# Kernel optimization log

Measured on AMD Instinct MI355X. Metric: run time of the kernel, lower is better.

The kernel has to match this reference:

```python
import jax, jax.numpy as jnp
import numpy as np

B, S, E, H = 2, 2048, 512, 8
D = E // H  # head_dim = 64


def setup_inputs() -> dict:
    key = jax.random.key(0)
    ks = jax.random.split(key, 10)
    sc = 1.0 / np.sqrt(E)
    x = jax.random.normal(ks[0], (B, S, E), dtype=jnp.float32)
    # parent index per node: tree_structure[b][parent[b,i]] contains i
    parent = jax.random.randint(ks[1], (B, S), 0, S, dtype=jnp.int32)
    Wp = jax.random.normal(ks[2], (E, E), dtype=jnp.float32) * sc
    bp = jnp.zeros((E,), dtype=jnp.float32)
    Wc = jax.random.normal(ks[3], (E, E), dtype=jnp.float32) * sc
    bc = jnp.zeros((E,), dtype=jnp.float32)
    Ws = jax.random.normal(ks[4], (E, E), dtype=jnp.float32) * sc
    bs = jnp.zeros((E,), dtype=jnp.float32)
    Wo = jax.random.normal(ks[5], (E, E), dtype=jnp.float32) * sc
    bo = jnp.zeros((E,), dtype=jnp.float32)
    return {"x": x, "parent": parent, "Wp": Wp, "bp": bp, "Wc": Wc,
            "bc": bc, "Ws": Ws, "bs": bs, "Wo": Wo, "bo": bo}


def _tree_mask(parent):
    # Vectorized equivalent of the per-batch scatter loop:
    # mask[b, p, c] = mask[b, c, p] = 1 for each (parent, child) edge.
    b_idx = jnp.arange(B)[:, None]
    rows = jnp.arange(S)[None, :]
    m = jnp.zeros((B, S, S), dtype=bool)
    m = m.at[b_idx, rows, parent].set(True)
    m = m.at[b_idx, parent, rows].set(True)
    return m  # (B, S, S), broadcast over heads


def reference(x, parent, Wp, bp, Wc, bc, Ws, bs, Wo, bo):
    # Tri-projection
    p = (x @ Wp + bp).reshape(B, S, H, D)
    c = (x @ Wc + bc).reshape(B, S, H, D)
    s = (x @ Ws + bs).reshape(B, S, H, D)
    scores = jnp.einsum('bnhd,bmhd->bnhm', p, c) / jnp.sqrt(jnp.float32(D))
    mask = _tree_mask(parent)  # (B, S, S)
    scores = jnp.where(mask[:, :, None, :], scores, -jnp.inf)
    attn = jax.nn.softmax(scores, axis=-1)  # dropout is identity (train=False)
    out = jnp.einsum('bnhm,bmhd->bnhd', attn, s).reshape(B, S, E)
    return out @ Wo + bo
```

## Files before the change

### kernel.cpp

```cpp
#include <hip/hip_runtime.h>
#include <hip/hip_bf16.h>

#define B_  2
#define S_  2048
#define E_  512
#define H_  8
#define D_  64
#define BS_ (B_ * S_)
#define N1_ 1536
#define K_  512

typedef __bf16 bf16x8 __attribute__((ext_vector_type(8)));
typedef float  f32x4  __attribute__((ext_vector_type(4)));
typedef unsigned short us8 __attribute__((ext_vector_type(8)));

__device__ __forceinline__ ushort f2bf(float f) {
    unsigned u = __float_as_uint(f);
    unsigned r = (u + 0x7FFFu + ((u >> 16) & 1u)) >> 16;
    return (ushort)r;
}
__device__ __forceinline__ float bf2f(ushort b) {
    return __uint_as_float(((unsigned)b) << 16);
}

__device__ __forceinline__ void gld_lds16(const ushort* g, ushort* l) {
    __builtin_amdgcn_global_load_lds(
        (const __attribute__((address_space(1))) unsigned int*)g,
        (__attribute__((address_space(3))) unsigned int*)l, 16, 0, 0);
}

__global__ __launch_bounds__(256) void gemm1_kernel(
    const float* __restrict__ x,
    const float* __restrict__ Wp, const float* __restrict__ Wc,
    const float* __restrict__ Ws,
    const float* __restrict__ bp, const float* __restrict__ bc,
    const float* __restrict__ bs,
    ushort* __restrict__ PCS) {
    constexpr int TM = 128, TN = 96, TK = 64, LDP = 72;
    __shared__ ushort As[TM][LDP];
    __shared__ ushort Bs[TN][LDP];

    const int tid  = threadIdx.x;
    const int lane = tid & 63;
    const int wave = tid >> 6;
    const int wm = wave >> 1, wn = wave & 1;
    const int row0 = blockIdx.y * TM;
    const int col0 = blockIdx.x * TN;

    f32x4 acc[4][3] = {};

    const int ar  = tid >> 4;
    const int ac4 = tid & 15;
    const int lrow = lane & 15;
    const int lk   = (lane >> 4) * 8;

    for (int kt = 0; kt < K_; kt += TK) {
        #pragma unroll
        for (int j = 0; j < 8; j++) {
            int row = j * 16 + ar;
            float4 v = *(const float4*)(x + (size_t)(row0 + row) * K_ + kt + ac4 * 4);
            ushort4 h;
            h.x = f2bf(v.x); h.y = f2bf(v.y); h.z = f2bf(v.z); h.w = f2bf(v.w);
            *(ushort4*)(&As[row][ac4 * 4]) = h;
        }
        #pragma unroll
        for (int rd = 0; rd < 2; rd++) {
            int pid = rd * 256 + tid;
            if (pid < 384) {
                int pk = pid / 24, pn = pid % 24;
                int gc = col0 + pn * 4;
                const float* Wseg = (gc < 512) ? (Wp + gc)
                                  : (gc < 1024) ? (Wc + gc - 512)
                                  : (Ws + gc - 1024);
                float4 r0 = *(const float4*)(Wseg + (size_t)(kt + pk * 4 + 0) * 512);
                float4 r1 = *(const float4*)(Wseg + (size_t)(kt + pk * 4 + 1) * 512);
                float4 r2 = *(const float4*)(Wseg + (size_t)(kt + pk * 4 + 2) * 512);
                float4 r3 = *(const float4*)(Wseg + (size_t)(kt + pk * 4 + 3) * 512);
                ushort4 h;
                h.x = f2bf(r0.x); h.y = f2bf(r1.x); h.z = f2bf(r2.x); h.w = f2bf(r3.x);
                *(ushort4*)(&Bs[pn * 4 + 0][pk * 4]) = h;
                h.x = f2bf(r0.y); h.y = f2bf(r1.y); h.z = f2bf(r2.y); h.w = f2bf(r3.y);
                *(ushort4*)(&Bs[pn * 4 + 1][pk * 4]) = h;
                h.x = f2bf(r0.z); h.y = f2bf(r1.z); h.z = f2bf(r2.z); h.w = f2bf(r3.z);
                *(ushort4*)(&Bs[pn * 4 + 2][pk * 4]) = h;
                h.x = f2bf(r0.w); h.y = f2bf(r1.w); h.z = f2bf(r2.w); h.w = f2bf(r3.w);
                *(ushort4*)(&Bs[pn * 4 + 3][pk * 4]) = h;
            }
        }
        __syncthreads();

        #pragma unroll
        for (int kk = 0; kk < TK; kk += 32) {
            bf16x8 af[4], bfr[3];
            #pragma unroll
            for (int i = 0; i < 4; i++)
                af[i] = *(const bf16x8*)(&As[wm * 64 + i * 16 + lrow][kk + lk]);
            #pragma unroll
            for (int j = 0; j < 3; j++)
                bfr[j] = *(const bf16x8*)(&Bs[wn * 48 + j * 16 + lrow][kk + lk]);
            #pragma unroll
            for (int i = 0; i < 4; i++)
                #pragma unroll
                for (int j = 0; j < 3; j++)
                    acc[i][j] = __builtin_amdgcn_mfma_f32_16x16x32_bf16(
                        af[i], bfr[j], acc[i][j], 0, 0, 0);
        }
        __syncthreads();
    }

    const int ccol = lane & 15;
    const int crow = (lane >> 4) * 4;
    #pragma unroll
    for (int j = 0; j < 3; j++) {
        int gcol = col0 + wn * 48 + j * 16 + ccol;
        float bias = (gcol < 512) ? bp[gcol]
                   : (gcol < 1024) ? bc[gcol - 512] : bs[gcol - 1024];
        #pragma unroll
        for (int i = 0; i < 4; i++) {
            int grow = row0 + wm * 64 + i * 16 + crow;
            #pragma unroll
            for (int rg = 0; rg < 4; rg++)
                PCS[(size_t)(grow + rg) * N1_ + gcol] = f2bf(acc[i][j][rg] + bias);
        }
    }
}

__global__ __launch_bounds__(256) void gemm2_kernel(
    const ushort* __restrict__ A,
    const float* __restrict__ Wo, const float* __restrict__ bo,
    float* __restrict__ out) {
    constexpr int TM = 64, TN = 64, TK = 64, LDP = 72;
    __shared__ ushort As[TM][TK];
    __shared__ ushort Bs[TN][LDP];

    const int tid  = threadIdx.x;
    const int lane = tid & 63;
    const int wave = tid >> 6;
    const int wm = wave >> 1, wn = wave & 1;
    const int row0 = blockIdx.y * TM;
    const int col0 = blockIdx.x * TN;

    f32x4 acc[2][2] = {};

    const int srow = lane >> 3;
    const int scol = (lane & 7) * 8;
    const int pk = tid >> 4, pn = tid & 15;
    const int lrow = lane & 15;
    const int lk   = (lane >> 4) * 8;

    for (int kt = 0; kt < K_; kt += TK) {
        const ushort* ga = A + (size_t)(row0 + wave * 16 + srow) * K_ + kt + scol;
        gld_lds16(ga,            &As[wave * 16 + 0][0]);
        gld_lds16(ga + 8 * K_,   &As[wave * 16 + 8][0]);

        {
            const float* Wseg = Wo + col0 + pn * 4;
            float4 r0 = *(const float4*)(Wseg + (size_t)(kt + pk * 4 + 0) * 512);
            float4 r1 = *(const float4*)(Wseg + (size_t)(kt + pk * 4 + 1) * 512);
            float4 r2 = *(const float4*)(Wseg + (size_t)(kt + pk * 4 + 2) * 512);
            float4 r3 = *(const float4*)(Wseg + (size_t)(kt + pk * 4 + 3) * 512);
            ushort4 h;
            h.x = f2bf(r0.x); h.y = f2bf(r1.x); h.z = f2bf(r2.x); h.w = f2bf(r3.x);
            *(ushort4*)(&Bs[pn * 4 + 0][pk * 4]) = h;
            h.x = f2bf(r0.y); h.y = f2bf(r1.y); h.z = f2bf(r2.y); h.w = f2bf(r3.y);
            *(ushort4*)(&Bs[pn * 4 + 1][pk * 4]) = h;
            h.x = f2bf(r0.z); h.y = f2bf(r1.z); h.z = f2bf(r2.z); h.w = f2bf(r3.z);
            *(ushort4*)(&Bs[pn * 4 + 2][pk * 4]) = h;
            h.x = f2bf(r0.w); h.y = f2bf(r1.w); h.z = f2bf(r2.w); h.w = f2bf(r3.w);
            *(ushort4*)(&Bs[pn * 4 + 3][pk * 4]) = h;
        }
        __syncthreads();

        #pragma unroll
        for (int kk = 0; kk < TK; kk += 32) {
            bf16x8 af[2], bfr[2];
            #pragma unroll
            for (int i = 0; i < 2; i++)
                af[i] = *(const bf16x8*)(&As[wm * 32 + i * 16 + lrow][kk + lk]);
            #pragma unroll
            for (int j = 0; j < 2; j++)
                bfr[j] = *(const bf16x8*)(&Bs[wn * 32 + j * 16 + lrow][kk + lk]);
            #pragma unroll
            for (int i = 0; i < 2; i++)
                #pragma unroll
                for (int j = 0; j < 2; j++)
                    acc[i][j] = __builtin_amdgcn_mfma_f32_16x16x32_bf16(
                        af[i], bfr[j], acc[i][j], 0, 0, 0);
        }
        __syncthreads();
    }

    const int ccol = lane & 15;
    const int crow = (lane >> 4) * 4;
    #pragma unroll
    for (int j = 0; j < 2; j++) {
        int gcol = col0 + wn * 32 + j * 16 + ccol;
        float bias = bo[gcol];
        #pragma unroll
        for (int i = 0; i < 2; i++) {
            int grow = row0 + wm * 32 + i * 16 + crow;
            #pragma unroll
            for (int rg = 0; rg < 4; rg++)
                out[(size_t)(grow + rg) * E_ + gcol] = acc[i][j][rg] + bias;
        }
    }
}

__global__ __launch_bounds__(256) void attn_gather_kernel(
    const ushort* __restrict__ PCS, const int* __restrict__ parent,
    ushort* __restrict__ attn) {
    int gtid = blockIdx.x * blockDim.x + threadIdx.x;
    int w    = gtid >> 6;
    int lane = gtid & 63;
    int bbase = ((w >> 11) << 11);
    int i  = w & (S_ - 1);
    int rp = bbase + parent[w];

    float pnf[8];
    {
        us8 p8 = *(const us8*)(PCS + (size_t)w * N1_ + lane * 8);
        #pragma unroll
        for (int j = 0; j < 8; j++) pnf[j] = bf2f(p8[j]);
    }

    float Z, av[8];
    {
        const ushort* rm = PCS + (size_t)rp * N1_;
        us8 c8 = *(const us8*)(rm + 512  + lane * 8);
        us8 s8 = *(const us8*)(rm + 1024 + lane * 8);
        float t = 0.f;
        #pragma unroll
        for (int j = 0; j < 8; j++) t += pnf[j] * bf2f(c8[j]);
        t += __shfl_xor(t, 1); t += __shfl_xor(t, 2); t += __shfl_xor(t, 4);
        float e = __expf(t * 0.125f);
        Z = e;
        #pragma unroll
        for (int j = 0; j < 8; j++) av[j] = e * bf2f(s8[j]);
    }

    for (int t0 = 0; t0 < S_; t0 += 256) {
        int4 pv = *(const int4*)(parent + bbase + t0 + lane * 4);
        int pc[4] = {pv.x, pv.y, pv.z, pv.w};
        #pragma unroll
        for (int jj = 0; jj < 4; jj++) {
            unsigned long long mask = __ballot(pc[jj] == i);
            while (mask) {
                int l = __ffsll(mask) - 1;
                mask &= mask - 1;
                int c = bbase + t0 + l * 4 + jj;
                if (c == rp) continue;
                const ushort* rc = PCS + (size_t)c * N1_;
                us8 c8 = *(const us8*)(rc + 512  + lane * 8);
                us8 s8 = *(const us8*)(rc + 1024 + lane * 8);
                float t = 0.f;
                #pragma unroll
                for (int j = 0; j < 8; j++) t += pnf[j] * bf2f(c8[j]);
                t += __shfl_xor(t, 1); t += __shfl_xor(t, 2); t += __shfl_xor(t, 4);
                float e = __expf(t * 0.125f);
                Z += e;
                #pragma unroll
                for (int j = 0; j < 8; j++) av[j] += e * bf2f(s8[j]);
            }
        }
    }

    float rz = 1.0f / Z;
    us8 o8;
    #pragma unroll
    for (int j = 0; j < 8; j++) o8[j] = f2bf(av[j] * rz);
    *(us8*)(attn + (size_t)w * E_ + lane * 8) = o8;
}

extern "C" void kernel_launch(void* const* d_in, const int* in_sizes, int n_in,
                              void* d_out, int out_size, void* d_ws, size_t ws_size,
                              hipStream_t stream) {
    const float* x      = (const float*)d_in[0];
    const int*   parent = (const int*)  d_in[1];
    const float* Wp     = (const float*)d_in[2];
    const float* bp     = (const float*)d_in[3];
    const float* Wc     = (const float*)d_in[4];
    const float* bc     = (const float*)d_in[5];
    const float* Ws     = (const float*)d_in[6];
    const float* bs     = (const float*)d_in[7];
    const float* Wo     = (const float*)d_in[8];
    const float* bo     = (const float*)d_in[9];
    float* out = (float*)d_out;

    char* ws = (char*)d_ws;
    ushort* PCS_bf  = (ushort*)(ws + 0);
    ushort* attn_bf = (ushort*)(ws + 12582912);

    gemm1_kernel<<<dim3(N1_ / 96, BS_ / 128), 256, 0, stream>>>(
        x, Wp, Wc, Ws, bp, bc, bs, PCS_bf);

    attn_gather_kernel<<<BS_ * 64 / 256, 256, 0, stream>>>(
        PCS_bf, parent, attn_bf);

    gemm2_kernel<<<dim3(E_ / 64, BS_ / 64), 256, 0, stream>>>(
        attn_bf, Wo, bo, out);
}
```

Baseline: 124.5 us.

## Fuse projection, tree attention and output GEMMs into one cooperative persistent kernel

Replaces the three kernel launches with a single cooperative kernel of 512 blocks that uses grid-wide syncs between phases. A new prologue converts x to bf16 and transposes all weights to bf16 once, so both GEMMs can load tiles straight to LDS with global_load_lds instead of doing per-tile float loads, conversion and transposed LDS writes. The intent is to remove launch gaps and the redundant weight conversion work. In exchange it adds an extra pass over x and the weights, three grid barriers, and a cooperative launch whose grid must fit on the device.

```diff
diff --git a/kernel.cpp b/kernel.cpp
--- a/kernel.cpp
+++ b/kernel.cpp
@@ -1,5 +1,8 @@
 #include <hip/hip_runtime.h>
 #include <hip/hip_bf16.h>
+#include <hip/hip_cooperative_groups.h>
+
+namespace cg = cooperative_groups;
 
 #define B_  2
 #define S_  2048
@@ -29,246 +32,236 @@
         (__attribute__((address_space(3))) unsigned int*)l, 16, 0, 0);
 }
 
-__global__ __launch_bounds__(256) void gemm1_kernel(
-    const float* __restrict__ x,
-    const float* __restrict__ Wp, const float* __restrict__ Wc,
-    const float* __restrict__ Ws,
-    const float* __restrict__ bp, const float* __restrict__ bc,
-    const float* __restrict__ bs,
-    ushort* __restrict__ PCS) {
-    constexpr int TM = 128, TN = 96, TK = 64, LDP = 72;
-    __shared__ ushort As[TM][LDP];
-    __shared__ ushort Bs[TN][LDP];
-
+__global__ __launch_bounds__(256, 2) void fused_kernel(
+    const float* __restrict__ x, const int* __restrict__ parent,
+    const float* __restrict__ Wp, const float* __restrict__ bp,
+    const float* __restrict__ Wc, const float* __restrict__ bc,
+    const float* __restrict__ Ws, const float* __restrict__ bs,
+    const float* __restrict__ Wo, const float* __restrict__ bo,
+    float* __restrict__ out,
+    ushort* __restrict__ x_bf, ushort* __restrict__ Wcat_t,
+    ushort* __restrict__ Wo_t, ushort* __restrict__ PCS,
+    ushort* __restrict__ attn) {
+    __shared__ ushort smem[14336];
+    cg::grid_group grid = cg::this_grid();
+
+    const int bx   = blockIdx.x;
     const int tid  = threadIdx.x;
     const int lane = tid & 63;
     const int wave = tid >> 6;
-    const int wm = wave >> 1, wn = wave & 1;
-    const int row0 = blockIdx.y * TM;
-    const int col0 = blockIdx.x * TN;
-
-    f32x4 acc[4][3] = {};
-
-    const int ar  = tid >> 4;
-    const int ac4 = tid & 15;
-    const int lrow = lane & 15;
-    const int lk   = (lane >> 4) * 8;
-
-    for (int kt = 0; kt < K_; kt += TK) {
+
+    {
+        int gtid = bx * 256 + tid;
         #pragma unroll
-        for (int j = 0; j < 8; j++) {
-            int row = j * 16 + ar;
-            float4 v = *(const float4*)(x + (size_t)(row0 + row) * K_ + kt + ac4 * 4);
-            ushort4 h;
-            h.x = f2bf(v.x); h.y = f2bf(v.y); h.z = f2bf(v.z); h.w = f2bf(v.w);
-            *(ushort4*)(&As[row][ac4 * 4]) = h;
-        }
+        for (int t = 0; t < 4; t++) {
+            int idx = t * 131072 + gtid;
+            float4 v = ((const float4*)x)[idx];
+            ushort4 o;
+            o.x = f2bf(v.x); o.y = f2bf(v.y); o.z = f2bf(v.z); o.w = f2bf(v.w);
+            ((ushort4*)x_bf)[idx] = o;
+        }
+        if (bx < 256) {
+            ushort (*T)[65] = (ushort(*)[65])smem;
+            int z = bx >> 6, t = bx & 63;
+            const float* src = (z == 0) ? Wp : (z == 1) ? Wc : (z == 2) ? Ws : Wo;
+            ushort* dst = (z < 3) ? (Wcat_t + (size_t)z * 512 * 512) : Wo_t;
+            int n0 = (t & 7) * 64, k0 = (t >> 3) * 64;
+            int g = tid >> 6, l = tid & 63;
+            #pragma unroll
+            for (int r = 0; r < 16; r++) {
+                int kk = g * 16 + r;
+                T[kk][l] = f2bf(src[(size_t)(k0 + kk) * 512 + n0 + l]);
+            }
+            __syncthreads();
+            #pragma unroll
+            for (int r = 0; r < 16; r++) {
+                int nn = g * 16 + r;
+                dst[(size_t)(n0 + nn) * 512 + k0 + l] = T[l][nn];
+            }
+        }
+    }
+    grid.sync();
+
+    {
+        ushort (*As)[64] = (ushort(*)[64])smem;
+        ushort (*Bs)[64] = (ushort(*)[64])(smem + 8192);
+        const int wm = wave >> 1, wn = wave & 1;
+        const int row0 = (bx >> 4) * 128;
+        const int col0 = (bx & 15) * 96;
+        f32x4 acc[4][3] = {};
+        const int srow = lane >> 3;
+        const int scol = (lane & 7) * 8;
+        const int lrow = lane & 15;
+        const int lk   = (lane >> 4) * 8;
+
+        for (int kt = 0; kt < K_; kt += 64) {
+            const ushort* ga = x_bf + (size_t)(row0 + wave * 32 + srow) * K_ + kt + scol;
+            #pragma unroll
+            for (int j = 0; j < 4; j++)
+                gld_lds16(ga + (size_t)j * 8 * K_, &As[wave * 32 + j * 8][0]);
+            const ushort* gb = Wcat_t + (size_t)(col0 + wave * 24 + srow) * K_ + kt + scol;
+            #pragma unroll
+            for (int j = 0; j < 3; j++)
+                gld_lds16(gb + (size_t)j * 8 * K_, &Bs[wave * 24 + j * 8][0]);
+            __syncthreads();
+
+            #pragma unroll
+            for (int kk = 0; kk < 64; kk += 32) {
+                bf16x8 af[4], bfr[3];
+                #pragma unroll
+                for (int i = 0; i < 4; i++)
+                    af[i] = *(const bf16x8*)(&As[wm * 64 + i * 16 + lrow][kk + lk]);
+                #pragma unroll
+                for (int j = 0; j < 3; j++)
+                    bfr[j] = *(const bf16x8*)(&Bs[wn * 48 + j * 16 + lrow][kk + lk]);
+                #pragma unroll
+                for (int i = 0; i < 4; i++)
+                    #pragma unroll
+                    for (int j = 0; j < 3; j++)
+                        acc[i][j] = __builtin_amdgcn_mfma_f32_16x16x32_bf16(
+                            af[i], bfr[j], acc[i][j], 0, 0, 0);
+            }
+            __syncthreads();
+        }
+
+        const int ccol = lane & 15;
+        const int crow = (lane >> 4) * 4;
         #pragma unroll
-        for (int rd = 0; rd < 2; rd++) {
-            int pid = rd * 256 + tid;
-            if (pid < 384) {
-                int pk = pid / 24, pn = pid % 24;
-                int gc = col0 + pn * 4;
-                const float* Wseg = (gc < 512) ? (Wp + gc)
-                                  : (gc < 1024) ? (Wc + gc - 512)
-                                  : (Ws + gc - 1024);
-                float4 r0 = *(const float4*)(Wseg + (size_t)(kt + pk * 4 + 0) * 512);
-                float4 r1 = *(const float4*)(Wseg + (size_t)(kt + pk * 4 + 1) * 512);
-                float4 r2 = *(const float4*)(Wseg + (size_t)(kt + pk * 4 + 2) * 512);
-                float4 r3 = *(const float4*)(Wseg + (size_t)(kt + pk * 4 + 3) * 512);
-                ushort4 h;
-                h.x = f2bf(r0.x); h.y = f2bf(r1.x); h.z = f2bf(r2.x); h.w = f2bf(r3.x);
-                *(ushort4*)(&Bs[pn * 4 + 0][pk * 4]) = h;
-                h.x = f2bf(r0.y); h.y = f2bf(r1.y); h.z = f2bf(r2.y); h.w = f2bf(r3.y);
-                *(ushort4*)(&Bs[pn * 4 + 1][pk * 4]) = h;
-                h.x = f2bf(r0.z); h.y = f2bf(r1.z); h.z = f2bf(r2.z); h.w = f2bf(r3.z);
-                *(ushort4*)(&Bs[pn * 4 + 2][pk * 4]) = h;
-                h.x = f2bf(r0.w); h.y = f2bf(r1.w); h.z = f2bf(r2.w); h.w = f2bf(r3.w);
-                *(ushort4*)(&Bs[pn * 4 + 3][pk * 4]) = h;
-            }
-        }
-        __syncthreads();
-
-        #pragma unroll
-        for (int kk = 0; kk < TK; kk += 32) {
-            bf16x8 af[4], bfr[3];
-            #pragma unroll
-            for (int i = 0; i < 4; i++)
-                af[i] = *(const bf16x8*)(&As[wm * 64 + i * 16 + lrow][kk + lk]);
-            #pragma unroll
-            for (int j = 0; j < 3; j++)
-                bfr[j] = *(const bf16x8*)(&Bs[wn * 48 + j * 16 + lrow][kk + lk]);
-            #pragma unroll
-            for (int i = 0; i < 4; i++)
-                #pragma unroll
-                for (int j = 0; j < 3; j++)
-                    acc[i][j] = __builtin_amdgcn_mfma_f32_16x16x32_bf16(
-                        af[i], bfr[j], acc[i][j], 0, 0, 0);
-        }
-        __syncthreads();
-    }
-
-    const int ccol = lane & 15;
-    const int crow = (lane >> 4) * 4;
-    #pragma unroll
-    for (int j = 0; j < 3; j++) {
-        int gcol = col0 + wn * 48 + j * 16 + ccol;
-        float bias = (gcol < 512) ? bp[gcol]
-                   : (gcol < 1024) ? bc[gcol - 512] : bs[gcol - 1024];
-        #pragma unroll
-        for (int i = 0; i < 4; i++) {
-            int grow = row0 + wm * 64 + i * 16 + crow;
-            #pragma unroll
-            for (int rg = 0; rg < 4; rg++)
-                PCS[(size_t)(grow + rg) * N1_ + gcol] = f2bf(acc[i][j][rg] + bias);
-        }
-    }
-}
-
-__global__ __launch_bounds__(256) void gemm2_kernel(
-    const ushort* __restrict__ A,
-    const float* __restrict__ Wo, const float* __restrict__ bo,
-    float* __restrict__ out) {
-    constexpr int TM = 64, TN = 64, TK = 64, LDP = 72;
-    __shared__ ushort As[TM][TK];
-    __shared__ ushort Bs[TN][LDP];
-
-    const int tid  = threadIdx.x;
-    const int lane = tid & 63;
-    const int wave = tid >> 6;
-    const int wm = wave >> 1, wn = wave & 1;
-    const int row0 = blockIdx.y * TM;
-    const int col0 = blockIdx.x * TN;
-
-    f32x4 acc[2][2] = {};
-
-    const int srow = lane >> 3;
-    const int scol = (lane & 7) * 8;
-    const int pk = tid >> 4, pn = tid & 15;
-    const int lrow = lane & 15;
-    const int lk   = (lane >> 4) * 8;
-
-    for (int kt = 0; kt < K_; kt += TK) {
-        const ushort* ga = A + (size_t)(row0 + wave * 16 + srow) * K_ + kt + scol;
-        gld_lds16(ga,            &As[wave * 16 + 0][0]);
-        gld_lds16(ga + 8 * K_,   &As[wave * 16 + 8][0]);
-
-        {
-            const float* Wseg = Wo + col0 + pn * 4;
-            float4 r0 = *(const float4*)(Wseg + (size_t)(kt + pk * 4 + 0) * 512);
-            float4 r1 = *(const float4*)(Wseg + (size_t)(kt + pk * 4 + 1) * 512);
-            float4 r2 = *(const float4*)(Wseg + (size_t)(kt + pk * 4 + 2) * 512);
-            float4 r3 = *(const float4*)(Wseg + (size_t)(kt + pk * 4 + 3) * 512);
-            ushort4 h;
-            h.x = f2bf(r0.x); h.y = f2bf(r1.x); h.z = f2bf(r2.x); h.w = f2bf(r3.x);
-            *(ushort4*)(&Bs[pn * 4 + 0][pk * 4]) = h;
-            h.x = f2bf(r0.y); h.y = f2bf(r1.y); h.z = f2bf(r2.y); h.w = f2bf(r3.y);
-            *(ushort4*)(&Bs[pn * 4 + 1][pk * 4]) = h;
-            h.x = f2bf(r0.z); h.y = f2bf(r1.z); h.z = f2bf(r2.z); h.w = f2bf(r3.z);
-            *(ushort4*)(&Bs[pn * 4 + 2][pk * 4]) = h;
-            h.x = f2bf(r0.w); h.y = f2bf(r1.w); h.z = f2bf(r2.w); h.w = f2bf(r3.w);
-            *(ushort4*)(&Bs[pn * 4 + 3][pk * 4]) = h;
-        }
-        __syncthreads();
-
-        #pragma unroll
-        for (int kk = 0; kk < TK; kk += 32) {
-            bf16x8 af[2], bfr[2];
-            #pragma unroll
-            for (int i = 0; i < 2; i++)
-                af[i] = *(const bf16x8*)(&As[wm * 32 + i * 16 + lrow][kk + lk]);
-            #pragma unroll
-            for (int j = 0; j < 2; j++)
-                bfr[j] = *(const bf16x8*)(&Bs[wn * 32 + j * 16 + lrow][kk + lk]);
-            #pragma unroll
-            for (int i = 0; i < 2; i++)
-                #pragma unroll
-                for (int j = 0; j < 2; j++)
-                    acc[i][j] = __builtin_amdgcn_mfma_f32_16x16x32_bf16(
-                        af[i], bfr[j], acc[i][j], 0, 0, 0);
-        }
-        __syncthreads();
-    }
-
-    const int ccol = lane & 15;
-    const int crow = (lane >> 4) * 4;
-    #pragma unroll
-    for (int j = 0; j < 2; j++) {
-        int gcol = col0 + wn * 32 + j * 16 + ccol;
-        float bias = bo[gcol];
-        #pragma unroll
-        for (int i = 0; i < 2; i++) {
-            int grow = row0 + wm * 32 + i * 16 + crow;
-            #pragma unroll
-            for (int rg = 0; rg < 4; rg++)
-                out[(size_t)(grow + rg) * E_ + gcol] = acc[i][j][rg] + bias;
-        }
-    }
-}
-
-__global__ __launch_bounds__(256) void attn_gather_kernel(
-    const ushort* __restrict__ PCS, const int* __restrict__ parent,
-    ushort* __restrict__ attn) {
-    int gtid = blockIdx.x * blockDim.x + threadIdx.x;
-    int w    = gtid >> 6;
-    int lane = gtid & 63;
-    int bbase = ((w >> 11) << 11);
-    int i  = w & (S_ - 1);
-    int rp = bbase + parent[w];
-
-    float pnf[8];
-    {
-        us8 p8 = *(const us8*)(PCS + (size_t)w * N1_ + lane * 8);
-        #pragma unroll
-        for (int j = 0; j < 8; j++) pnf[j] = bf2f(p8[j]);
-    }
-
-    float Z, av[8];
-    {
-        const ushort* rm = PCS + (size_t)rp * N1_;
-        us8 c8 = *(const us8*)(rm + 512  + lane * 8);
-        us8 s8 = *(const us8*)(rm + 1024 + lane * 8);
-        float t = 0.f;
-        #pragma unroll
-        for (int j = 0; j < 8; j++) t += pnf[j] * bf2f(c8[j]);
-        t += __shfl_xor(t, 1); t += __shfl_xor(t, 2); t += __shfl_xor(t, 4);
-        float e = __expf(t * 0.125f);
-        Z = e;
-        #pragma unroll
-        for (int j = 0; j < 8; j++) av[j] = e * bf2f(s8[j]);
-    }
-
-    for (int t0 = 0; t0 < S_; t0 += 256) {
-        int4 pv = *(const int4*)(parent + bbase + t0 + lane * 4);
-        int pc[4] = {pv.x, pv.y, pv.z, pv.w};
-        #pragma unroll
-        for (int jj = 0; jj < 4; jj++) {
-            unsigned long long mask = __ballot(pc[jj] == i);
-            while (mask) {
-                int l = __ffsll(mask) - 1;
-                mask &= mask - 1;
-                int c = bbase + t0 + l * 4 + jj;
-                if (c == rp) continue;
-                const ushort* rc = PCS + (size_t)c * N1_;
-                us8 c8 = *(const us8*)(rc + 512  + lane * 8);
-                us8 s8 = *(const us8*)(rc + 1024 + lane * 8);
+        for (int j = 0; j < 3; j++) {
+            int gcol = col0 + wn * 48 + j * 16 + ccol;
+            float bias = (gcol < 512) ? bp[gcol]
+                       : (gcol < 1024) ? bc[gcol - 512] : bs[gcol - 1024];
+            #pragma unroll
+            for (int i = 0; i < 4; i++) {
+                int grow = row0 + wm * 64 + i * 16 + crow;
+                #pragma unroll
+                for (int rg = 0; rg < 4; rg++)
+                    PCS[(size_t)(grow + rg) * N1_ + gcol] = f2bf(acc[i][j][rg] + bias);
+            }
+        }
+    }
+    grid.sync();
+
+    {
+        int wid = bx * 4 + wave;
+        for (int r = 0; r < 2; r++) {
+            int w = wid * 2 + r;
+            int bbase = ((w >> 11) << 11);
+            int i  = w & (S_ - 1);
+            int rp = bbase + parent[w];
+
+            float pnf[8];
+            {
+                us8 p8 = *(const us8*)(PCS + (size_t)w * N1_ + lane * 8);
+                #pragma unroll
+                for (int j = 0; j < 8; j++) pnf[j] = bf2f(p8[j]);
+            }
+
+            float Z, av[8];
+            {
+                const ushort* rm = PCS + (size_t)rp * N1_;
+                us8 c8 = *(const us8*)(rm + 512  + lane * 8);
+                us8 s8 = *(const us8*)(rm + 1024 + lane * 8);
                 float t = 0.f;
                 #pragma unroll
                 for (int j = 0; j < 8; j++) t += pnf[j] * bf2f(c8[j]);
                 t += __shfl_xor(t, 1); t += __shfl_xor(t, 2); t += __shfl_xor(t, 4);
                 float e = __expf(t * 0.125f);
-                Z += e;
-                #pragma unroll
-                for (int j = 0; j < 8; j++) av[j] += e * bf2f(s8[j]);
-            }
-        }
-    }
-
-    float rz = 1.0f / Z;
-    us8 o8;
-    #pragma unroll
-    for (int j = 0; j < 8; j++) o8[j] = f2bf(av[j] * rz);
-    *(us8*)(attn + (size_t)w * E_ + lane * 8) = o8;
+                Z = e;
+                #pragma unroll
+                for (int j = 0; j < 8; j++) av[j] = e * bf2f(s8[j]);
+            }
+
+            for (int t0 = 0; t0 < S_; t0 += 256) {
+                int4 pv = *(const int4*)(parent + bbase + t0 + lane * 4);
+                int pc[4] = {pv.x, pv.y, pv.z, pv.w};
+                #pragma unroll
+                for (int jj = 0; jj < 4; jj++) {
+                    unsigned long long mask = __ballot(pc[jj] == i);
+                    while (mask) {
+                        int l = __ffsll(mask) - 1;
+                        mask &= mask - 1;
+                        int c = bbase + t0 + l * 4 + jj;
+                        if (c == rp) continue;
+                        const ushort* rc = PCS + (size_t)c * N1_;
+                        us8 c8 = *(const us8*)(rc + 512  + lane * 8);
+                        us8 s8 = *(const us8*)(rc + 1024 + lane * 8);
+                        float t = 0.f;
+                        #pragma unroll
+                        for (int j = 0; j < 8; j++) t += pnf[j] * bf2f(c8[j]);
+                        t += __shfl_xor(t, 1); t += __shfl_xor(t, 2); t += __shfl_xor(t, 4);
+                        float e = __expf(t * 0.125f);
+                        Z += e;
+                        #pragma unroll
+                        for (int j = 0; j < 8; j++) av[j] += e * bf2f(s8[j]);
+                    }
+                }
+            }
+
+            float rz = 1.0f / Z;
+            us8 o8;
+            #pragma unroll
+            for (int j = 0; j < 8; j++) o8[j] = f2bf(av[j] * rz);
+            *(us8*)(attn + (size_t)w * E_ + lane * 8) = o8;
+        }
+    }
+    grid.sync();
+
+    {
+        ushort (*As2)[64] = (ushort(*)[64])smem;
+        ushort (*Bs2)[64] = (ushort(*)[64])(smem + 4096);
+        const int wm = wave >> 1, wn = wave & 1;
+        const int row0 = (bx >> 3) * 64;
+        const int col0 = (bx & 7) * 64;
+        f32x4 acc[2][2] = {};
+        const int srow = lane >> 3;
+        const int scol = (lane & 7) * 8;
+        const int lrow = lane & 15;
+        const int lk   = (lane >> 4) * 8;
+
+        for (int kt = 0; kt < K_; kt += 64) {
+            const ushort* ga = attn + (size_t)(row0 + wave * 16 + srow) * K_ + kt + scol;
+            gld_lds16(ga,           &As2[wave * 16 + 0][0]);
+            gld_lds16(ga + 8 * K_,  &As2[wave * 16 + 8][0]);
+            const ushort* gb = Wo_t + (size_t)(col0 + wave * 16 + srow) * K_ + kt + scol;
+            gld_lds16(gb,           &Bs2[wave * 16 + 0][0]);
+            gld_lds16(gb + 8 * K_,  &Bs2[wave * 16 + 8][0]);
+            __syncthreads();
+
+            #pragma unroll
+            for (int kk = 0; kk < 64; kk += 32) {
+                bf16x8 af[2], bfr[2];
+                #pragma unroll
+                for (int i = 0; i < 2; i++)
+                    af[i] = *(const bf16x8*)(&As2[wm * 32 + i * 16 + lrow][kk + lk]);
+                #pragma unroll
+                for (int j = 0; j < 2; j++)
+                    bfr[j] = *(const bf16x8*)(&Bs2[wn * 32 + j * 16 + lrow][kk + lk]);
+                #pragma unroll
+                for (int i = 0; i < 2; i++)
+                    #pragma unroll
+                    for (int j = 0; j < 2; j++)
+                        acc[i][j] = __builtin_amdgcn_mfma_f32_16x16x32_bf16(
+                            af[i], bfr[j], acc[i][j], 0, 0, 0);
+            }
+            __syncthreads();
+        }
+
+        const int ccol = lane & 15;
+        const int crow = (lane >> 4) * 4;
+        #pragma unroll
+        for (int j = 0; j < 2; j++) {
+            int gcol = col0 + wn * 32 + j * 16 + ccol;
+            float bias = bo[gcol];
+            #pragma unroll
+            for (int i = 0; i < 2; i++) {
+                int grow = row0 + wm * 32 + i * 16 + crow;
+                #pragma unroll
+                for (int rg = 0; rg < 4; rg++)
+                    out[(size_t)(grow + rg) * E_ + gcol] = acc[i][j][rg] + bias;
+            }
+        }
+    }
 }
 
 extern "C" void kernel_launch(void* const* d_in, const int* in_sizes, int n_in,
@@ -287,15 +280,20 @@
     float* out = (float*)d_out;
 
     char* ws = (char*)d_ws;
-    ushort* PCS_bf  = (ushort*)(ws + 0);
-    ushort* attn_bf = (ushort*)(ws + 12582912);
-
-    gemm1_kernel<<<dim3(N1_ / 96, BS_ / 128), 256, 0, stream>>>(
-        x, Wp, Wc, Ws, bp, bc, bs, PCS_bf);
-
-    attn_gather_kernel<<<BS_ * 64 / 256, 256, 0, stream>>>(
-        PCS_bf, parent, attn_bf);
-
-    gemm2_kernel<<<dim3(E_ / 64, BS_ / 64), 256, 0, stream>>>(
-        attn_bf, Wo, bo, out);
-}
+    ushort* x_bf    = (ushort*)(ws + 0);
+    ushort* Wcat_t  = (ushort*)(ws + 4194304);
+    ushort* Wo_t    = (ushort*)(ws + 5767168);
+    ushort* PCS_bf  = (ushort*)(ws + 6291456);
+    ushort* attn_bf = (ushort*)(ws + 18874368);
+
+    void* args[] = {
+        (void*)&x, (void*)&parent,
+        (void*)&Wp, (void*)&bp, (void*)&Wc, (void*)&bc,
+        (void*)&Ws, (void*)&bs, (void*)&Wo, (void*)&bo,
+        (void*)&out,
+        (void*)&x_bf, (void*)&Wcat_t, (void*)&Wo_t,
+        (void*)&PCS_bf, (void*)&attn_bf,
+    };
+    hipLaunchCooperativeKernel((void*)fused_kernel, dim3(512), dim3(256),
+                               args, 0, stream);
+}
```

New measurement: 321.7 us. 158% more time.
